# Kernel optimization log

Hardware: AMD Instinct MI355X
Metric: run time of the kernel (lower is better)

## Reference

```python
import jax, jax.numpy as jnp
import numpy as np

V, E, H = 128, 100, 1024  # vocab_size, embedding_dim, rnn_units
B, T = 64, 512


def setup_inputs() -> dict:
    key = jax.random.key(0)
    ks = jax.random.split(key, 8)
    tokens = jax.random.randint(ks[0], (B, T), 0, V, dtype=jnp.int32)
    emb = jax.random.normal(ks[1], (V, E), dtype=jnp.float32) * 0.05
    Wx = jax.random.normal(ks[2], (E, 3 * H), dtype=jnp.float32) * (1.0 / np.sqrt(E))
    Uh = jax.random.normal(ks[3], (H, 3 * H), dtype=jnp.float32) * (1.0 / np.sqrt(H))
    b_in = jnp.zeros((3 * H,), dtype=jnp.float32)   # input bias (Keras reset_after has 2 biases)
    b_rec = jnp.zeros((3 * H,), dtype=jnp.float32)  # recurrent bias
    Wd = jax.random.normal(ks[4], (H, V), dtype=jnp.float32) * (1.0 / np.sqrt(H))
    bd = jnp.zeros((V,), dtype=jnp.float32)
    return {"tokens": tokens, "emb": emb, "Wx": Wx, "Uh": Uh,
            "b_in": b_in, "b_rec": b_rec, "Wd": Wd, "bd": bd}


def _gru_seq(x, Wx, Uh, b_in, b_rec):
    # x: [B, T, E] -> hidden sequence [B, T, H]. Keras GRU, reset_after=True,
    # gate order [z | r | h], recurrent_activation=sigmoid, activation=relu.
    xp = jnp.einsum('bte,eh->bth', x, Wx) + b_in  # [B, T, 3H], all input projections fused
    xp_t = jnp.swapaxes(xp, 0, 1)                 # [T, B, 3H]

    def step(h, xt):
        rec = h @ Uh + b_rec                      # [B, 3H]
        xz, xr, xh = xt[:, :H], xt[:, H:2 * H], xt[:, 2 * H:]
        rz, rr, rh = rec[:, :H], rec[:, H:2 * H], rec[:, 2 * H:]
        z = jax.nn.sigmoid(xz + rz)
        r = jax.nn.sigmoid(xr + rr)
        hh = jax.nn.relu(xh + r * rh)             # reset applied after recurrent matmul
        h_new = z * h + (1.0 - z) * hh
        return h_new, h_new

    h0 = jnp.zeros((x.shape[0], H), dtype=x.dtype)
    _, hs = jax.lax.scan(step, h0, xp_t)
    return jnp.swapaxes(hs, 0, 1)                 # [B, T, H]


def reference(tokens, emb, Wx, Uh, b_in, b_rec, Wd, bd):
    x = emb[tokens]                               # [B, T, E] embedding lookup
    seq = _gru_seq(x, Wx, Uh, b_in, b_rec)        # [B, T, H]
    logits = jnp.einsum('bth,hv->btv', seq, Wd) + bd  # [B, T, V]
    return logits
```

## Files before the change

### kernel.cpp

```cpp
#include <hip/hip_runtime.h>
#include <stdint.h>

constexpr int kV = 128, kE = 100, kH = 1024, kB = 64, kT = 512, kH3 = 3072;

typedef __bf16 bf16_t;
typedef __bf16 bf16x8 __attribute__((ext_vector_type(8)));
typedef float f32x4 __attribute__((ext_vector_type(4)));
typedef unsigned int u32;
typedef unsigned long long u64;

__global__ void k_prep_P(const float* __restrict__ emb, const float* __restrict__ Wx,
                         const float* __restrict__ b_in, const float* __restrict__ b_rec,
                         float* __restrict__ P) {
    const int n = blockIdx.x * 256 + threadIdx.x;
    const int v0 = blockIdx.y * 32;
    float wcol[kE];
#pragma unroll
    for (int e = 0; e < kE; ++e) wcol[e] = Wx[e * kH3 + n];
    const float bias = b_in[n] + (n < 2 * kH ? b_rec[n] : 0.f);
    for (int vi = 0; vi < 32; ++vi) {
        const int v = v0 + vi;
        float acc = bias;
#pragma unroll
        for (int e = 0; e < kE; ++e) acc += emb[v * kE + e] * wcol[e];
        P[v * kH3 + n] = acc;
    }
}

__global__ void k_prep_WdT(const float* __restrict__ Wd, bf16_t* __restrict__ WdT) {
    const int i = blockIdx.x * 256 + threadIdx.x;
    const int v = i & 127, k = i >> 7;
    WdT[v * kH + k] = (bf16_t)Wd[k * kV + v];
}

__launch_bounds__(512, 1)
__global__ void k_scan(const int* __restrict__ tokens, const float* __restrict__ Uh,
                       const float* __restrict__ Pg, const float* __restrict__ b_rec,
                       bf16_t* __restrict__ hbuf, bf16_t* __restrict__ seq,
                       unsigned* __restrict__ flags) {
    __shared__ float Pl[kV][104];
    __shared__ float part[2][8][8][104];
    const int tid = threadIdx.x;
    const int g = blockIdx.x >> 5, slot = blockIdx.x & 31;
    const int c0 = slot * 32;
    const int lane = tid & 63, wave = tid >> 6;
    const int r16 = lane & 15, grp = lane >> 4;

    for (int idx = tid; idx < kV * 96; idx += 512) {
        const int v = idx / 96, gi = idx % 96;
        const int col = (gi >> 5) * kH + c0 + (gi & 31);
        Pl[v][gi] = Pg[v * kH3 + col];
    }
    bf16x8 bf[6][4];
#pragma unroll
    for (int tile = 0; tile < 6; ++tile) {
        const int col = (tile >> 1) * kH + c0 + (tile & 1) * 16 + r16;
#pragma unroll
        for (int ks = 0; ks < 4; ++ks)
#pragma unroll
            for (int j = 0; j < 8; ++j)
                bf[tile][ks][j] = (bf16_t)Uh[(wave * 128 + ks * 32 + grp * 8 + j) * kH3 + col];
    }
    const int c4 = (lane & 7) * 4;
    const int myrow = 8 * g + wave;
    float brh4[4], hreg[4] = {0.f, 0.f, 0.f, 0.f};
#pragma unroll
    for (int i = 0; i < 4; ++i) brh4[i] = b_rec[2 * kH + c0 + c4 + i];
    int tokc = tokens[(size_t)myrow * kT + 0];
    const int arow = r16 & 7;
    __syncthreads();

    for (int t = 0; t < kT; ++t) {
        if (t > 0) {
            if (lane < 32) {
                const unsigned* fp = flags +
                    (((size_t)g * 32 + (wave * 4 + (lane >> 3))) * 8 + (lane & 7)) * 32;
                long guard = 0;
                while (__hip_atomic_load(fp, __ATOMIC_RELAXED, __HIP_MEMORY_SCOPE_AGENT)
                       < (unsigned)t) {
                    __builtin_amdgcn_s_sleep(1);
                    if (++guard > (1L << 15)) break;
                }
            }
            f32x4 acc[6];
#pragma unroll
            for (int tl = 0; tl < 6; ++tl) acc[tl] = (f32x4){0.f, 0.f, 0.f, 0.f};
            const bf16_t* hprev = hbuf + (((t & 1) ^ 1) * kB + 8 * g) * kH;
            const u64* ap = (const u64*)(hprev + arow * kH + wave * 128 + grp * 8);
            bf16x8 av[4];
#pragma unroll
            for (int ks = 0; ks < 4; ++ks) {
                union { u64 u[2]; bf16x8 v; } au;
                au.u[0] = __hip_atomic_load(ap + ks * 8, __ATOMIC_RELAXED,
                                            __HIP_MEMORY_SCOPE_AGENT);
                au.u[1] = __hip_atomic_load(ap + ks * 8 + 1, __ATOMIC_RELAXED,
                                            __HIP_MEMORY_SCOPE_AGENT);
                av[ks] = au.v;
            }
#pragma unroll
            for (int ks = 0; ks < 4; ++ks)
#pragma unroll
                for (int tl = 0; tl < 6; ++tl)
                    acc[tl] = __builtin_amdgcn_mfma_f32_16x16x32_bf16(av[ks], bf[tl][ks],
                                                                      acc[tl], 0, 0, 0);
            if (grp < 2) {
#pragma unroll
                for (int tl = 0; tl < 6; ++tl)
#pragma unroll
                    for (int q = 0; q < 4; ++q)
                        part[t & 1][wave][grp * 4 + q][tl * 16 + r16] = acc[tl][q];
            }
        }
        __syncthreads();

        f32x4 rz = {0.f, 0.f, 0.f, 0.f}, rr = rz, rh = rz;
        if (t > 0) {
#pragma unroll
            for (int w2 = 0; w2 < 8; ++w2) {
                rz += *(const f32x4*)&part[t & 1][w2][wave][c4];
                rr += *(const f32x4*)&part[t & 1][w2][wave][32 + c4];
                rh += *(const f32x4*)&part[t & 1][w2][wave][64 + c4];
            }
        }
        unsigned short hs[4];
#pragma unroll
        for (int i = 0; i < 4; ++i) {
            const float z = 1.f / (1.f + __expf(-(Pl[tokc][c4 + i] + rz[i])));
            const float r = 1.f / (1.f + __expf(-(Pl[tokc][32 + c4 + i] + rr[i])));
            float hh = Pl[tokc][64 + c4 + i] + r * (rh[i] + brh4[i]);
            hh = hh > 0.f ? hh : 0.f;
            const float hnew = z * hreg[i] + (1.f - z) * hh;
            hreg[i] = hnew;
            union { bf16_t h; unsigned short s; } cv; cv.h = (bf16_t)hnew;
            hs[i] = cv.s;
        }
        const u64 hp = (u64)hs[0] | ((u64)hs[1] << 16) | ((u64)hs[2] << 32) | ((u64)hs[3] << 48);
        if (t < kT - 1) {
            if (lane < 8)
                __hip_atomic_store((u64*)(hbuf + (((t & 1) * kB) + myrow) * kH + c0 + c4),
                                   hp, __ATOMIC_RELAXED, __HIP_MEMORY_SCOPE_AGENT);
            asm volatile("s_waitcnt vmcnt(0)" ::: "memory");
            if (lane == 0)
                __hip_atomic_store(flags + (((size_t)g * 32 + slot) * 8 + wave) * 32,
                                   (unsigned)(t + 1),
                                   __ATOMIC_RELAXED, __HIP_MEMORY_SCOPE_AGENT);
        }
        if (lane < 8)
            *(u64*)(seq + ((size_t)myrow * kT + t) * kH + c0 + c4) = hp;
        if (t < kT - 1) tokc = tokens[(size_t)myrow * kT + t + 1];
    }
}

__global__ void k_logits(const bf16_t* __restrict__ seq, const bf16_t* __restrict__ WdT,
                         const float* __restrict__ bd, float* __restrict__ out) {
    const int m0 = blockIdx.x * 64;
    const int lane = threadIdx.x & 63, wave = threadIdx.x >> 6;
    const int r16 = lane & 15, grp = lane >> 4;
    f32x4 acc[8];
#pragma unroll
    for (int n = 0; n < 8; ++n) acc[n] = (f32x4){0.f, 0.f, 0.f, 0.f};
    const bf16_t* ap = seq + (m0 + 16 * wave + r16) * kH + 8 * grp;
    const bf16_t* bp = WdT + r16 * kH + 8 * grp;
    for (int ks = 0; ks < 32; ++ks) {
        const int k0 = 32 * ks;
        bf16x8 a = *(const bf16x8*)(ap + k0);
#pragma unroll
        for (int nt = 0; nt < 8; ++nt) {
            bf16x8 b = *(const bf16x8*)(bp + nt * 16 * kH + k0);
            acc[nt] = __builtin_amdgcn_mfma_f32_16x16x32_bf16(a, b, acc[nt], 0, 0, 0);
        }
    }
#pragma unroll
    for (int nt = 0; nt < 8; ++nt) {
        const int v = 16 * nt + r16;
        const float bias = bd[v];
#pragma unroll
        for (int q = 0; q < 4; ++q) {
            const int m = m0 + 16 * wave + 4 * grp + q;
            out[m * kV + v] = acc[nt][q] + bias;
        }
    }
}

extern "C" void kernel_launch(void* const* d_in, const int* in_sizes, int n_in,
                              void* d_out, int out_size, void* d_ws, size_t ws_size,
                              hipStream_t stream) {
    const int*   tokens = (const int*)d_in[0];
    const float* emb    = (const float*)d_in[1];
    const float* Wx     = (const float*)d_in[2];
    const float* Uh     = (const float*)d_in[3];
    const float* b_in   = (const float*)d_in[4];
    const float* b_rec  = (const float*)d_in[5];
    const float* Wd     = (const float*)d_in[6];
    const float* bd     = (const float*)d_in[7];
    float* out = (float*)d_out;

    char* ws = (char*)d_ws;
    bf16_t*   seq   = (bf16_t*)ws;
    float*    P     = (float*)(ws + 67108864);
    bf16_t*   WdT   = (bf16_t*)(ws + 68681728);
    bf16_t*   hbuf  = (bf16_t*)(ws + 68943872);
    unsigned* flags = (unsigned*)(ws + 69206016);

    k_prep_P<<<dim3(12, 4), 256, 0, stream>>>(emb, Wx, b_in, b_rec, P);
    k_prep_WdT<<<512, 256, 0, stream>>>(Wd, WdT);
    hipMemsetAsync(flags, 0, 262144, stream);
    k_scan<<<256, 512, 0, stream>>>(tokens, Uh, P, b_rec, hbuf, seq, flags);
    k_logits<<<512, 256, 0, stream>>>(seq, WdT, bd, out);
}
```

Baseline: 2.658 ms.

## Embed step tags in hidden-state words to replace separate flag synchronization

```diff
diff --git a/kernel.cpp b/kernel.cpp
--- a/kernel.cpp
+++ b/kernel.cpp
@@ -36,8 +36,7 @@
 __launch_bounds__(512, 1)
 __global__ void k_scan(const int* __restrict__ tokens, const float* __restrict__ Uh,
                        const float* __restrict__ Pg, const float* __restrict__ b_rec,
-                       bf16_t* __restrict__ hbuf, bf16_t* __restrict__ seq,
-                       unsigned* __restrict__ flags) {
+                       u32* __restrict__ hsig, bf16_t* __restrict__ seq) {
     __shared__ float Pl[kV][104];
     __shared__ float part[2][8][8][104];
     const int tid = threadIdx.x;
@@ -72,37 +71,44 @@
 
     for (int t = 0; t < kT; ++t) {
         if (t > 0) {
-            if (lane < 32) {
-                const unsigned* fp = flags +
-                    (((size_t)g * 32 + (wave * 4 + (lane >> 3))) * 8 + (lane & 7)) * 32;
+            const u32 tag = (u32)t;
+            const u32* hpar = hsig + (size_t)(((t - 1) & 1) * kB + 8 * g + arow) * kH;
+            f32x4 acc[6];
+#pragma unroll
+            for (int tl = 0; tl < 6; ++tl) acc[tl] = (f32x4){0.f, 0.f, 0.f, 0.f};
+#pragma unroll
+            for (int ks = 0; ks < 4; ++ks) {
+                const u64* bp = (const u64*)(hpar + wave * 128 + ks * 32 + grp * 8);
+                u64 q0, q1, q2, q3;
                 long guard = 0;
-                while (__hip_atomic_load(fp, __ATOMIC_RELAXED, __HIP_MEMORY_SCOPE_AGENT)
-                       < (unsigned)t) {
+                for (;;) {
+                    q0 = __hip_atomic_load(bp, __ATOMIC_RELAXED, __HIP_MEMORY_SCOPE_AGENT);
+                    if (((u32)q0 & 0xffffu) == tag && ((u32)(q0 >> 32) & 0xffffu) == tag) break;
                     __builtin_amdgcn_s_sleep(1);
                     if (++guard > (1L << 15)) break;
                 }
+                guard = 0;
+                for (;;) {
+                    q1 = __hip_atomic_load(bp + 1, __ATOMIC_RELAXED, __HIP_MEMORY_SCOPE_AGENT);
+                    q2 = __hip_atomic_load(bp + 2, __ATOMIC_RELAXED, __HIP_MEMORY_SCOPE_AGENT);
+                    q3 = __hip_atomic_load(bp + 3, __ATOMIC_RELAXED, __HIP_MEMORY_SCOPE_AGENT);
+                    const bool ok = ((u32)q1 & 0xffffu) == tag && ((u32)(q1 >> 32) & 0xffffu) == tag
+                                 && ((u32)q2 & 0xffffu) == tag && ((u32)(q2 >> 32) & 0xffffu) == tag
+                                 && ((u32)q3 & 0xffffu) == tag && ((u32)(q3 >> 32) & 0xffffu) == tag;
+                    if (ok) break;
+                    __builtin_amdgcn_s_sleep(1);
+                    if (++guard > (1L << 12)) break;
+                }
+                union { u32 w[4]; bf16x8 v; } uv;
+                uv.w[0] = ((u32)q0 >> 16) | ((u32)(q0 >> 32) & 0xffff0000u);
+                uv.w[1] = ((u32)q1 >> 16) | ((u32)(q1 >> 32) & 0xffff0000u);
+                uv.w[2] = ((u32)q2 >> 16) | ((u32)(q2 >> 32) & 0xffff0000u);
+                uv.w[3] = ((u32)q3 >> 16) | ((u32)(q3 >> 32) & 0xffff0000u);
+#pragma unroll
+                for (int tl = 0; tl < 6; ++tl)
+                    acc[tl] = __builtin_amdgcn_mfma_f32_16x16x32_bf16(uv.v, bf[tl][ks],
+                                                                      acc[tl], 0, 0, 0);
             }
-            f32x4 acc[6];
-#pragma unroll
-            for (int tl = 0; tl < 6; ++tl) acc[tl] = (f32x4){0.f, 0.f, 0.f, 0.f};
-            const bf16_t* hprev = hbuf + (((t & 1) ^ 1) * kB + 8 * g) * kH;
-            const u64* ap = (const u64*)(hprev + arow * kH + wave * 128 + grp * 8);
-            bf16x8 av[4];
-#pragma unroll
-            for (int ks = 0; ks < 4; ++ks) {
-                union { u64 u[2]; bf16x8 v; } au;
-                au.u[0] = __hip_atomic_load(ap + ks * 8, __ATOMIC_RELAXED,
-                                            __HIP_MEMORY_SCOPE_AGENT);
-                au.u[1] = __hip_atomic_load(ap + ks * 8 + 1, __ATOMIC_RELAXED,
-                                            __HIP_MEMORY_SCOPE_AGENT);
-                av[ks] = au.v;
-            }
-#pragma unroll
-            for (int ks = 0; ks < 4; ++ks)
-#pragma unroll
-                for (int tl = 0; tl < 6; ++tl)
-                    acc[tl] = __builtin_amdgcn_mfma_f32_16x16x32_bf16(av[ks], bf[tl][ks],
-                                                                      acc[tl], 0, 0, 0);
             if (grp < 2) {
 #pragma unroll
                 for (int tl = 0; tl < 6; ++tl)
@@ -134,19 +140,21 @@
             union { bf16_t h; unsigned short s; } cv; cv.h = (bf16_t)hnew;
             hs[i] = cv.s;
         }
-        const u64 hp = (u64)hs[0] | ((u64)hs[1] << 16) | ((u64)hs[2] << 32) | ((u64)hs[3] << 48);
-        if (t < kT - 1) {
-            if (lane < 8)
-                __hip_atomic_store((u64*)(hbuf + (((t & 1) * kB) + myrow) * kH + c0 + c4),
-                                   hp, __ATOMIC_RELAXED, __HIP_MEMORY_SCOPE_AGENT);
-            asm volatile("s_waitcnt vmcnt(0)" ::: "memory");
-            if (lane == 0)
-                __hip_atomic_store(flags + (((size_t)g * 32 + slot) * 8 + wave) * 32,
-                                   (unsigned)(t + 1),
-                                   __ATOMIC_RELAXED, __HIP_MEMORY_SCOPE_AGENT);
-        }
-        if (lane < 8)
-            *(u64*)(seq + ((size_t)myrow * kT + t) * kH + c0 + c4) = hp;
+        if (t < kT - 1 && lane < 8) {
+            const u32 tg = (u32)(t + 1);
+            u64* dst = (u64*)(hsig + (size_t)((t & 1) * kB + myrow) * kH + c0 + c4);
+            const u64 lo = ((u64)(tg | ((u32)hs[0] << 16)))
+                         | (((u64)(tg | ((u32)hs[1] << 16))) << 32);
+            const u64 hi = ((u64)(tg | ((u32)hs[2] << 16)))
+                         | (((u64)(tg | ((u32)hs[3] << 16))) << 32);
+            __hip_atomic_store(dst,     lo, __ATOMIC_RELAXED, __HIP_MEMORY_SCOPE_AGENT);
+            __hip_atomic_store(dst + 1, hi, __ATOMIC_RELAXED, __HIP_MEMORY_SCOPE_AGENT);
+        }
+        if (lane < 8) {
+            const u64 sq = (u64)hs[0] | ((u64)hs[1] << 16) | ((u64)hs[2] << 32)
+                         | ((u64)hs[3] << 48);
+            *(u64*)(seq + ((size_t)myrow * kT + t) * kH + c0 + c4) = sq;
+        }
         if (t < kT - 1) tokc = tokens[(size_t)myrow * kT + t + 1];
     }
 }
@@ -196,15 +204,14 @@
     float* out = (float*)d_out;
 
     char* ws = (char*)d_ws;
-    bf16_t*   seq   = (bf16_t*)ws;
-    float*    P     = (float*)(ws + 67108864);
-    bf16_t*   WdT   = (bf16_t*)(ws + 68681728);
-    bf16_t*   hbuf  = (bf16_t*)(ws + 68943872);
-    unsigned* flags = (unsigned*)(ws + 69206016);
+    bf16_t* seq  = (bf16_t*)ws;
+    float*  P    = (float*)(ws + 67108864);
+    bf16_t* WdT  = (bf16_t*)(ws + 68681728);
+    u32*    hsig = (u32*)(ws + 68943872);
 
     k_prep_P<<<dim3(12, 4), 256, 0, stream>>>(emb, Wx, b_in, b_rec, P);
     k_prep_WdT<<<512, 256, 0, stream>>>(Wd, WdT);
-    hipMemsetAsync(flags, 0, 262144, stream);
-    k_scan<<<256, 512, 0, stream>>>(tokens, Uh, P, b_rec, hbuf, seq, flags);
+    hipMemsetAsync(hsig, 0, 524288, stream);
+    k_scan<<<256, 512, 0, stream>>>(tokens, Uh, P, b_rec, hsig, seq);
     k_logits<<<512, 256, 0, stream>>>(seq, WdT, bd, out);
 }
```

Measured after the change: 3.328 ms. +25.2%, slower.

## Repartition GRU scan to 16 batch rows by 16 columns per block

Applied to the files above, without the earlier changes.

```diff
diff --git a/kernel.cpp b/kernel.cpp
--- a/kernel.cpp
+++ b/kernel.cpp
@@ -38,43 +38,43 @@
                        const float* __restrict__ Pg, const float* __restrict__ b_rec,
                        bf16_t* __restrict__ hbuf, bf16_t* __restrict__ seq,
                        unsigned* __restrict__ flags) {
-    __shared__ float Pl[kV][104];
-    __shared__ float part[2][8][8][104];
+    __shared__ float Pl[kV][52];
+    __shared__ float part[2][8][16][52];
     const int tid = threadIdx.x;
-    const int g = blockIdx.x >> 5, slot = blockIdx.x & 31;
-    const int c0 = slot * 32;
+    const int g = blockIdx.x >> 6, slot = blockIdx.x & 63;
+    const int c0 = slot * 16;
     const int lane = tid & 63, wave = tid >> 6;
     const int r16 = lane & 15, grp = lane >> 4;
 
-    for (int idx = tid; idx < kV * 96; idx += 512) {
-        const int v = idx / 96, gi = idx % 96;
-        const int col = (gi >> 5) * kH + c0 + (gi & 31);
+    for (int idx = tid; idx < kV * 48; idx += 512) {
+        const int v = idx / 48, gi = idx % 48;
+        const int col = (gi >> 4) * kH + c0 + (gi & 15);
         Pl[v][gi] = Pg[v * kH3 + col];
     }
-    bf16x8 bf[6][4];
-#pragma unroll
-    for (int tile = 0; tile < 6; ++tile) {
-        const int col = (tile >> 1) * kH + c0 + (tile & 1) * 16 + r16;
+    bf16x8 bf[3][4];
+#pragma unroll
+    for (int tl = 0; tl < 3; ++tl) {
+        const int col = tl * kH + c0 + r16;
 #pragma unroll
         for (int ks = 0; ks < 4; ++ks)
 #pragma unroll
             for (int j = 0; j < 8; ++j)
-                bf[tile][ks][j] = (bf16_t)Uh[(wave * 128 + ks * 32 + grp * 8 + j) * kH3 + col];
-    }
-    const int c4 = (lane & 7) * 4;
-    const int myrow = 8 * g + wave;
-    float brh4[4], hreg[4] = {0.f, 0.f, 0.f, 0.f};
-#pragma unroll
-    for (int i = 0; i < 4; ++i) brh4[i] = b_rec[2 * kH + c0 + c4 + i];
-    int tokc = tokens[(size_t)myrow * kT + 0];
-    const int arow = r16 & 7;
+                bf[tl][ks][j] = (bf16_t)Uh[(wave * 128 + ks * 32 + grp * 8 + j) * kH3 + col];
+    }
+    const int rowL = 2 * wave + ((lane >> 3) & 1);
+    const int gr = 16 * g + rowL;
+    const int cp = (lane & 7) * 2;
+    float brh[2], hreg[2] = {0.f, 0.f};
+    brh[0] = b_rec[2 * kH + c0 + cp];
+    brh[1] = b_rec[2 * kH + c0 + cp + 1];
+    int tokc = (lane < 16) ? tokens[(size_t)gr * kT + 0] : 0;
     __syncthreads();
 
     for (int t = 0; t < kT; ++t) {
         if (t > 0) {
-            if (lane < 32) {
+            {
                 const unsigned* fp = flags +
-                    (((size_t)g * 32 + (wave * 4 + (lane >> 3))) * 8 + (lane & 7)) * 32;
+                    (((size_t)g * 64 + (8 * wave + (lane >> 3))) * 8 + (lane & 7)) * 32;
                 long guard = 0;
                 while (__hip_atomic_load(fp, __ATOMIC_RELAXED, __HIP_MEMORY_SCOPE_AGENT)
                        < (unsigned)t) {
@@ -82,11 +82,8 @@
                     if (++guard > (1L << 15)) break;
                 }
             }
-            f32x4 acc[6];
-#pragma unroll
-            for (int tl = 0; tl < 6; ++tl) acc[tl] = (f32x4){0.f, 0.f, 0.f, 0.f};
-            const bf16_t* hprev = hbuf + (((t & 1) ^ 1) * kB + 8 * g) * kH;
-            const u64* ap = (const u64*)(hprev + arow * kH + wave * 128 + grp * 8);
+            const bf16_t* hprev = hbuf + (((t & 1) ^ 1) * kB + 16 * g + r16) * kH;
+            const u64* ap = (const u64*)(hprev + wave * 128 + grp * 8);
             bf16x8 av[4];
 #pragma unroll
             for (int ks = 0; ks < 4; ++ks) {
@@ -97,57 +94,72 @@
                                             __HIP_MEMORY_SCOPE_AGENT);
                 av[ks] = au.v;
             }
+            f32x4 acc[3];
+#pragma unroll
+            for (int tl = 0; tl < 3; ++tl) acc[tl] = (f32x4){0.f, 0.f, 0.f, 0.f};
 #pragma unroll
             for (int ks = 0; ks < 4; ++ks)
 #pragma unroll
-                for (int tl = 0; tl < 6; ++tl)
+                for (int tl = 0; tl < 3; ++tl)
                     acc[tl] = __builtin_amdgcn_mfma_f32_16x16x32_bf16(av[ks], bf[tl][ks],
                                                                       acc[tl], 0, 0, 0);
-            if (grp < 2) {
-#pragma unroll
-                for (int tl = 0; tl < 6; ++tl)
-#pragma unroll
-                    for (int q = 0; q < 4; ++q)
-                        part[t & 1][wave][grp * 4 + q][tl * 16 + r16] = acc[tl][q];
-            }
+#pragma unroll
+            for (int tl = 0; tl < 3; ++tl)
+#pragma unroll
+                for (int q = 0; q < 4; ++q)
+                    part[t & 1][wave][grp * 4 + q][tl * 16 + r16] = acc[tl][q];
         }
         __syncthreads();
 
-        f32x4 rz = {0.f, 0.f, 0.f, 0.f}, rr = rz, rh = rz;
-        if (t > 0) {
-#pragma unroll
-            for (int w2 = 0; w2 < 8; ++w2) {
-                rz += *(const f32x4*)&part[t & 1][w2][wave][c4];
-                rr += *(const f32x4*)&part[t & 1][w2][wave][32 + c4];
-                rh += *(const f32x4*)&part[t & 1][w2][wave][64 + c4];
-            }
-        }
-        unsigned short hs[4];
-#pragma unroll
-        for (int i = 0; i < 4; ++i) {
-            const float z = 1.f / (1.f + __expf(-(Pl[tokc][c4 + i] + rz[i])));
-            const float r = 1.f / (1.f + __expf(-(Pl[tokc][32 + c4 + i] + rr[i])));
-            float hh = Pl[tokc][64 + c4 + i] + r * (rh[i] + brh4[i]);
-            hh = hh > 0.f ? hh : 0.f;
-            const float hnew = z * hreg[i] + (1.f - z) * hh;
-            hreg[i] = hnew;
-            union { bf16_t h; unsigned short s; } cv; cv.h = (bf16_t)hnew;
-            hs[i] = cv.s;
-        }
-        const u64 hp = (u64)hs[0] | ((u64)hs[1] << 16) | ((u64)hs[2] << 32) | ((u64)hs[3] << 48);
+        unsigned short hs[2];
+        if (lane < 16) {
+            float2 rz = {0.f, 0.f}, rr = rz, rh = rz;
+            if (t > 0) {
+#pragma unroll
+                for (int w2 = 0; w2 < 8; ++w2) {
+                    const float* pr = &part[t & 1][w2][rowL][0];
+                    const float2 a = *(const float2*)(pr + cp);
+                    const float2 b = *(const float2*)(pr + 16 + cp);
+                    const float2 c = *(const float2*)(pr + 32 + cp);
+                    rz.x += a.x; rz.y += a.y;
+                    rr.x += b.x; rr.y += b.y;
+                    rh.x += c.x; rh.y += c.y;
+                }
+            }
+            const float2 pz = *(const float2*)&Pl[tokc][cp];
+            const float2 pr2 = *(const float2*)&Pl[tokc][16 + cp];
+            const float2 ph = *(const float2*)&Pl[tokc][32 + cp];
+#pragma unroll
+            for (int i = 0; i < 2; ++i) {
+                const float xz = i ? pz.y : pz.x, xr = i ? pr2.y : pr2.x, xh = i ? ph.y : ph.x;
+                const float az = i ? rz.y : rz.x, ar = i ? rr.y : rr.x, ah = i ? rh.y : rh.x;
+                const float z = 1.f / (1.f + __expf(-(xz + az)));
+                const float r = 1.f / (1.f + __expf(-(xr + ar)));
+                float hh = xh + r * (ah + brh[i]);
+                hh = hh > 0.f ? hh : 0.f;
+                const float hnew = z * hreg[i] + (1.f - z) * hh;
+                hreg[i] = hnew;
+                union { bf16_t h; unsigned short s; } cv; cv.h = (bf16_t)hnew;
+                hs[i] = cv.s;
+            }
+            if (t < kT - 1) {
+                const u32 hp = (u32)hs[0] | ((u32)hs[1] << 16);
+                __hip_atomic_store((u32*)(hbuf + (((t & 1) * kB) + gr) * kH + c0 + cp),
+                                   hp, __ATOMIC_RELAXED, __HIP_MEMORY_SCOPE_AGENT);
+            }
+        }
         if (t < kT - 1) {
-            if (lane < 8)
-                __hip_atomic_store((u64*)(hbuf + (((t & 1) * kB) + myrow) * kH + c0 + c4),
-                                   hp, __ATOMIC_RELAXED, __HIP_MEMORY_SCOPE_AGENT);
             asm volatile("s_waitcnt vmcnt(0)" ::: "memory");
             if (lane == 0)
-                __hip_atomic_store(flags + (((size_t)g * 32 + slot) * 8 + wave) * 32,
+                __hip_atomic_store(flags + (((size_t)g * 64 + slot) * 8 + wave) * 32,
                                    (unsigned)(t + 1),
                                    __ATOMIC_RELAXED, __HIP_MEMORY_SCOPE_AGENT);
         }
-        if (lane < 8)
-            *(u64*)(seq + ((size_t)myrow * kT + t) * kH + c0 + c4) = hp;
-        if (t < kT - 1) tokc = tokens[(size_t)myrow * kT + t + 1];
+        if (lane < 16) {
+            *(u32*)(seq + ((size_t)gr * kT + t) * kH + c0 + cp) =
+                (u32)hs[0] | ((u32)hs[1] << 16);
+            if (t < kT - 1) tokc = tokens[(size_t)gr * kT + t + 1];
+        }
     }
 }
 
```

After: 3.075 ms. 1.16x slower.
